# Optimization experiments

Hardware: AMD Instinct MI355X
Metric: run time of the kernel (lower is better)

## Reference

```python
import jax, jax.numpy as jnp
import numpy as np

LOG2_HASHMAP_SIZE = 19
HASHMAP_MASK = np.uint32((1 << LOG2_HASHMAP_SIZE) - 1)
# num_mf_layers=4 -> mf_layer_indices=[2,5,8,11] of the 12-level geometric
# resolution list between base=16 and finest=512
RESOLUTIONS = (30, 80, 210, 512)
PRIMES = (np.uint32(1), np.uint32(11614769), np.uint32(2654435761))
N_POINTS = 2_000_000
N_FEATS = 2

# 8 corner offsets of a 3D voxel, shape [8, 3]
CORNER_OFFSETS = jnp.array([[i, j, k] for i in (0, 1) for j in (0, 1) for k in (0, 1)], dtype=jnp.int32)


def _hash3(coords):
    # coords: [..., 3] int32 grid coordinates -> [...] int32 hash index
    c = coords.astype(jnp.uint32)
    h = (c[..., 0] * PRIMES[0]) ^ (c[..., 1] * PRIMES[1]) ^ (c[..., 2] * PRIMES[2])
    return (h & HASHMAP_MASK).astype(jnp.int32)


def setup_inputs() -> dict:
    key = jax.random.key(0)
    k1, k2 = jax.random.split(key)
    # points inside the unit bounding box
    x = jax.random.uniform(k1, (N_POINTS, 3), dtype=jnp.float32)
    # 4 hash tables, init U(-1e-4, 1e-4) as in nn.init.uniform_
    tables = jax.random.uniform(k2, (len(RESOLUTIONS), 1 << LOG2_HASHMAP_SIZE, N_FEATS),
                                minval=-1e-4, maxval=1e-4, dtype=jnp.float32)
    return {"x": x, "tables": tables}


def reference(x, tables):
    # x: [N, 3] in [0, 1]; tables: [L, 2^19, F]
    outs = []
    for li, res in enumerate(RESOLUTIONS):
        scaled = x * jnp.float32(res)          # [N, 3]
        bottom = jnp.floor(scaled)             # voxel min vertex
        t = scaled - bottom                    # relative position in voxel, [N, 3]
        corners = bottom.astype(jnp.int32)[:, None, :] + CORNER_OFFSETS[None]  # [N, 8, 3]
        idx = _hash3(corners)                  # [N, 8]
        emb = tables[li][idx]                  # gather corner embeddings, [N, 8, F]
        # trilinear weights: prod over dims of (t if offset==1 else 1-t)
        w = jnp.where(CORNER_OFFSETS[None].astype(bool), t[:, None, :], 1.0 - t[:, None, :]).prod(axis=-1)  # [N, 8]
        outs.append(jnp.einsum('nc,ncf->nf', w, emb))  # [N, F]
    return jnp.concatenate(outs, axis=-1)  # [N, L*F] = [N, 8]
```

## Files before the change

### kernel.cpp

```cpp
#include <hip/hip_runtime.h>
#include <hip/hip_fp16.h>
#include <stdint.h>

#define LOG2_HASHMAP_SIZE 19
#define HASHMAP_SIZE (1u << LOG2_HASHMAP_SIZE)
#define HASHMAP_MASK (HASHMAP_SIZE - 1u)
#define N_LEVELS 4

#define R0 31
#define DENSE0_N (R0 * R0 * R0)
#define DENSE0_BYTES (DENSE0_N * 4)

typedef float v4f __attribute__((ext_vector_type(4)));

__device__ __forceinline__ uint32_t hash3(uint32_t ix, uint32_t iy, uint32_t iz) {
    return (ix ^ (iy * 11614769u) ^ (iz * 2654435761u)) & HASHMAP_MASK;
}

__device__ __forceinline__ float2 h2f(uint32_t p) {
    return __half22float2(*(const __half2*)&p);
}
__device__ __forceinline__ uint32_t f2h(float a, float b) {
    const __half2 p = __floats2half2_rn(a, b);
    return *(const uint32_t*)&p;
}

__device__ __forceinline__ float2 level_embed_p(float px, float py, float pz,
                                                const float* __restrict__ tables,
                                                int li, float r)
{
    const uint32_t P1 = 11614769u;
    const uint32_t P2 = 2654435761u;

    const float sx = px * r, sy = py * r, sz = pz * r;
    const float bx = floorf(sx), by = floorf(sy), bz = floorf(sz);
    const float tx = sx - bx, ty = sy - by, tz = sz - bz;
    const float ux = 1.0f - tx, uy = 1.0f - ty, uz = 1.0f - tz;

    const uint32_t ix = (uint32_t)(int)bx;
    const uint32_t iy = (uint32_t)(int)by;
    const uint32_t iz = (uint32_t)(int)bz;

    const uint32_t hy0 = iy * P1, hy1 = (iy + 1u) * P1;
    const uint32_t hz0 = iz * P2, hz1 = (iz + 1u) * P2;

    uint32_t S[4];
    float W[4];
    S[0] = hy0 ^ hz0;  W[0] = uy * uz;
    S[1] = hy0 ^ hz1;  W[1] = uy * tz;
    S[2] = hy1 ^ hz0;  W[2] = ty * uz;
    S[3] = hy1 ^ hz1;  W[3] = ty * tz;

    const float* tab = tables + (size_t)li * HASHMAP_SIZE * 2;
    const float2* __restrict__ tab2 = (const float2*)tab;

    float f0 = 0.0f, f1 = 0.0f;
    #pragma unroll
    for (int c = 0; c < 4; ++c) {
        const uint32_t h0 = (ix ^ S[c]) & HASHMAP_MASK;
        const uint32_t h1 = ((ix + 1u) ^ S[c]) & HASHMAP_MASK;
        const float2 e0 = tab2[h0];
        const float2 e1 = tab2[h1];
        f0 += W[c] * (ux * e0.x + tx * e1.x);
        f1 += W[c] * (ux * e0.y + tx * e1.y);
    }
    return make_float2(f0, f1);
}

__device__ __forceinline__ float2 level_embed_h16(float px, float py, float pz,
                                                  const uint32_t* __restrict__ t16,
                                                  float r)
{
    const uint32_t P1 = 11614769u;
    const uint32_t P2 = 2654435761u;

    const float sx = px * r, sy = py * r, sz = pz * r;
    const float bx = floorf(sx), by = floorf(sy), bz = floorf(sz);
    const float tx = sx - bx, ty = sy - by, tz = sz - bz;
    const float ux = 1.0f - tx, uy = 1.0f - ty, uz = 1.0f - tz;

    const uint32_t ix = (uint32_t)(int)bx;
    const uint32_t iy = (uint32_t)(int)by;
    const uint32_t iz = (uint32_t)(int)bz;

    const uint32_t hy0 = iy * P1, hy1 = (iy + 1u) * P1;
    const uint32_t hz0 = iz * P2, hz1 = (iz + 1u) * P2;

    uint32_t S[4];
    float W[4];
    S[0] = hy0 ^ hz0;  W[0] = uy * uz;
    S[1] = hy0 ^ hz1;  W[1] = uy * tz;
    S[2] = hy1 ^ hz0;  W[2] = ty * uz;
    S[3] = hy1 ^ hz1;  W[3] = ty * tz;

    const uint32_t D = ix ^ (ix + 1u);

    float f0 = 0.0f, f1 = 0.0f;
    if (D == 1u) {
        #pragma unroll
        for (int c = 0; c < 4; ++c) {
            const uint32_t h0 = (ix ^ S[c]) & HASHMAP_MASK;
            const uint2 v = ((const uint2*)t16)[h0 >> 1];
            const uint32_t p0 = (h0 & 1u) ? v.y : v.x;
            const uint32_t p1 = (h0 & 1u) ? v.x : v.y;
            const float2 e0 = h2f(p0);
            const float2 e1 = h2f(p1);
            f0 += W[c] * (ux * e0.x + tx * e1.x);
            f1 += W[c] * (ux * e0.y + tx * e1.y);
        }
    } else if (D == 3u) {
        #pragma unroll
        for (int c = 0; c < 4; ++c) {
            const uint32_t h0 = (ix ^ S[c]) & HASHMAP_MASK;
            const uint32_t b = h0 & ~3u;
            const uint4 v = *(const uint4*)(t16 + b);
            const uint32_t i0 = h0 & 3u;
            const uint32_t s01 = (i0 & 1u) ? v.y : v.x;
            const uint32_t s23 = (i0 & 1u) ? v.w : v.z;
            const uint32_t p0  = (i0 & 2u) ? s23 : s01;
            const uint32_t r01 = (i0 & 1u) ? v.z : v.w;
            const uint32_t r23 = (i0 & 1u) ? v.x : v.y;
            const uint32_t p1  = (i0 & 2u) ? r23 : r01;
            const float2 e0 = h2f(p0);
            const float2 e1 = h2f(p1);
            f0 += W[c] * (ux * e0.x + tx * e1.x);
            f1 += W[c] * (ux * e0.y + tx * e1.y);
        }
    } else {
        #pragma unroll
        for (int c = 0; c < 4; ++c) {
            const uint32_t h0 = (ix ^ S[c]) & HASHMAP_MASK;
            const uint32_t h1 = h0 ^ D;
            const float2 e0 = h2f(t16[h0]);
            const float2 e1 = h2f(t16[h1]);
            f0 += W[c] * (ux * e0.x + tx * e1.x);
            f1 += W[c] * (ux * e0.y + tx * e1.y);
        }
    }
    return make_float2(f0, f1);
}

__global__ __launch_bounds__(256) void convert_fp16(
    const float* __restrict__ tables, uint32_t* __restrict__ t16)
{
    const int i = blockIdx.x * blockDim.x + threadIdx.x;
    if (i >= 3 * (int)HASHMAP_SIZE) return;
    const float2 e = ((const float2*)tables)[HASHMAP_SIZE + i];
    t16[i] = f2h(e.x, e.y);
}

__global__ __launch_bounds__(256) void build_dense0(
    const float* __restrict__ tables, uint32_t* __restrict__ dense0)
{
    const int v = blockIdx.x * blockDim.x + threadIdx.x;
    if (v >= DENSE0_N) return;
    const int vx = v / (R0 * R0);
    const int rem = v - vx * (R0 * R0);
    const int vy = rem / R0;
    const int vz = rem - vy * R0;
    const uint32_t h = hash3((uint32_t)vx, (uint32_t)vy, (uint32_t)vz);
    const float2 e = ((const float2*)tables)[h];
    dense0[v] = f2h(e.x, e.y);
}

__global__ __launch_bounds__(256) void pass_hash(
    const float* __restrict__ x, const uint32_t* __restrict__ t16,
    uint32_t* __restrict__ ws, float r, int n)
{
    const int i = blockIdx.x * blockDim.x + threadIdx.x;
    if (i >= n) return;
    const float px = __builtin_nontemporal_load(x + 3 * (size_t)i + 0);
    const float py = __builtin_nontemporal_load(x + 3 * (size_t)i + 1);
    const float pz = __builtin_nontemporal_load(x + 3 * (size_t)i + 2);
    const float2 e = level_embed_h16(px, py, pz, t16, r);
    __builtin_nontemporal_store(f2h(e.x, e.y), ws + i);
}

extern __shared__ uint32_t s_dense[];

__global__ __launch_bounds__(1024) void final16_kernel(
    const float* __restrict__ x, const uint32_t* __restrict__ t16_l3,
    const uint32_t* __restrict__ dense0,
    const uint32_t* __restrict__ ws1, const uint32_t* __restrict__ ws2,
    float* __restrict__ out, int n)
{
    for (int i = threadIdx.x; i < DENSE0_N; i += 1024)
        s_dense[i] = dense0[i];
    __syncthreads();

    const size_t stride = (size_t)gridDim.x * 1024;
    for (size_t i = (size_t)blockIdx.x * 1024 + threadIdx.x; i < (size_t)n; i += stride) {
        const float px = __builtin_nontemporal_load(x + 3 * i + 0);
        const float py = __builtin_nontemporal_load(x + 3 * i + 1);
        const float pz = __builtin_nontemporal_load(x + 3 * i + 2);

        const float2 e3 = level_embed_h16(px, py, pz, t16_l3, 512.0f);

        const float sx = px * 30.0f, sy = py * 30.0f, sz = pz * 30.0f;
        const float bx = floorf(sx), by = floorf(sy), bz = floorf(sz);
        const float tx = sx - bx, ty = sy - by, tz = sz - bz;
        const float uxv = 1.0f - tx, uyv = 1.0f - ty, uzv = 1.0f - tz;
        const int ix = (int)bx, iy = (int)by, iz = (int)bz;
        const int lin = (ix * R0 + iy) * R0 + iz;

        float f0 = 0.0f, f1 = 0.0f;
        #pragma unroll
        for (int dx = 0; dx < 2; ++dx) {
            const float wx = dx ? tx : uxv;
            #pragma unroll
            for (int dy = 0; dy < 2; ++dy) {
                const float wxy = wx * (dy ? ty : uyv);
                const int base = lin + (dx * R0 + dy) * R0;
                const float2 c0 = h2f(s_dense[base]);
                const float2 c1 = h2f(s_dense[base + 1]);
                f0 += wxy * (uzv * c0.x + tz * c1.x);
                f1 += wxy * (uzv * c0.y + tz * c1.y);
            }
        }

        const float2 e1 = h2f(__builtin_nontemporal_load(ws1 + i));
        const float2 e2 = h2f(__builtin_nontemporal_load(ws2 + i));

        v4f* op = (v4f*)(out + 8 * i);
        v4f lo = {f0, f1, e1.x, e1.y};
        v4f hi = {e2.x, e2.y, e3.x, e3.y};
        __builtin_nontemporal_store(lo, op);
        __builtin_nontemporal_store(hi, op + 1);
    }
}

__global__ __launch_bounds__(256) void pass_direct_kernel(
    const float* __restrict__ x, const float* __restrict__ tables,
    float* __restrict__ out, int li, float r, int n)
{
    const int i = blockIdx.x * blockDim.x + threadIdx.x;
    if (i >= n) return;
    const float px = x[3 * (size_t)i + 0];
    const float py = x[3 * (size_t)i + 1];
    const float pz = x[3 * (size_t)i + 2];
    const float2 e = level_embed_p(px, py, pz, tables, li, r);
    float2* op = (float2*)(out + 8 * (size_t)i + 2 * li);
    *op = e;
}

extern "C" void kernel_launch(void* const* d_in, const int* in_sizes, int n_in,
                              void* d_out, int out_size, void* d_ws, size_t ws_size,
                              hipStream_t stream) {
    const float* x = (const float*)d_in[0];
    const float* tables = (const float*)d_in[1];
    float* out = (float*)d_out;
    const int n = in_sizes[0] / 3;

    const size_t t16_bytes = 3 * (size_t)HASHMAP_SIZE * 4;
    const size_t off_d0    = t16_bytes;
    const size_t off_ws1   = off_d0 + DENSE0_BYTES;
    const size_t off_ws2   = off_ws1 + (size_t)n * 4;
    const size_t ws_needed = off_ws2 + (size_t)n * 4;

    bool fused_ok = (ws_size >= ws_needed);
    if (fused_ok) {
        static int attr_ok = -1;
        if (attr_ok < 0) {
            attr_ok = (hipFuncSetAttribute(
                           reinterpret_cast<const void*>(final16_kernel),
                           hipFuncAttributeMaxDynamicSharedMemorySize,
                           DENSE0_BYTES) == hipSuccess) ? 1 : 0;
        }
        fused_ok = (attr_ok == 1);
    }

    if (fused_ok) {
        char* wsb = (char*)d_ws;
        uint32_t* t16    = (uint32_t*)wsb;
        uint32_t* dense0 = (uint32_t*)(wsb + off_d0);
        uint32_t* ws1    = (uint32_t*)(wsb + off_ws1);
        uint32_t* ws2    = (uint32_t*)(wsb + off_ws2);

        convert_fp16<<<(3 * HASHMAP_SIZE + 255) / 256, 256, 0, stream>>>(tables, t16);
        build_dense0<<<(DENSE0_N + 255) / 256, 256, 0, stream>>>(tables, dense0);

        const int block = 256;
        const int grid = (n + block - 1) / block;
        pass_hash<<<grid, block, 0, stream>>>(x, t16, ws1, 80.0f, n);
        pass_hash<<<grid, block, 0, stream>>>(x, t16 + HASHMAP_SIZE, ws2, 210.0f, n);
        final16_kernel<<<256, 1024, DENSE0_BYTES, stream>>>(
            x, t16 + 2 * HASHMAP_SIZE, dense0, ws1, ws2, out, n);
    } else {
        const float res[N_LEVELS] = {30.0f, 80.0f, 210.0f, 512.0f};
        const int block = 256;
        const int grid = (n + block - 1) / block;
        for (int li = 0; li < N_LEVELS; ++li) {
            pass_direct_kernel<<<grid, block, 0, stream>>>(
                x, tables, out, li, res[li], n);
        }
    }
}
```

Baseline: 239.4 us.

## Merge setup kernels, read level-0 dense grid from global, simplify hash-pair loads

The two table-preparation kernels become one launch. The final kernel no longer copies the 119 KB level-0 dense grid into LDS per block; it reads it from global/L2 with paired 8-byte loads and runs as a plain 256-thread grid instead of a persistent 1024-thread grid. The hashed-level corner lookup drops the 4-wide vector path and splits only on ix parity, fetching an adjacent pair in one load when ix is even. This removes the per-block LDS fill and its occupancy limit, at the cost of L2 traffic for the dense grid and separate loads in the odd-ix case.

New measurement: 253.3 us. +5.8%, slower.

```diff
diff --git a/kernel.cpp b/kernel.cpp
--- a/kernel.cpp
+++ b/kernel.cpp
@@ -11,6 +11,8 @@
 #define DENSE0_N (R0 * R0 * R0)
 #define DENSE0_BYTES (DENSE0_N * 4)
 
+#define CONV_N (3 * (int)HASHMAP_SIZE)
+
 typedef float v4f __attribute__((ext_vector_type(4)));
 
 __device__ __forceinline__ uint32_t hash3(uint32_t ix, uint32_t iy, uint32_t iz) {
@@ -23,6 +25,12 @@
 __device__ __forceinline__ uint32_t f2h(float a, float b) {
     const __half2 p = __floats2half2_rn(a, b);
     return *(const uint32_t*)&p;
+}
+
+__device__ __forceinline__ uint2 load8u(const uint32_t* p) {
+    uint2 v;
+    __builtin_memcpy(&v, p, 8);
+    return v;
 }
 
 __device__ __forceinline__ float2 level_embed_p(float px, float py, float pz,
@@ -93,10 +101,8 @@
     S[2] = hy1 ^ hz0;  W[2] = ty * uz;
     S[3] = hy1 ^ hz1;  W[3] = ty * tz;
 
-    const uint32_t D = ix ^ (ix + 1u);
-
     float f0 = 0.0f, f1 = 0.0f;
-    if (D == 1u) {
+    if ((ix & 1u) == 0u) {
         #pragma unroll
         for (int c = 0; c < 4; ++c) {
             const uint32_t h0 = (ix ^ S[c]) & HASHMAP_MASK;
@@ -108,29 +114,11 @@
             f0 += W[c] * (ux * e0.x + tx * e1.x);
             f1 += W[c] * (ux * e0.y + tx * e1.y);
         }
-    } else if (D == 3u) {
-        #pragma unroll
-        for (int c = 0; c < 4; ++c) {
-            const uint32_t h0 = (ix ^ S[c]) & HASHMAP_MASK;
-            const uint32_t b = h0 & ~3u;
-            const uint4 v = *(const uint4*)(t16 + b);
-            const uint32_t i0 = h0 & 3u;
-            const uint32_t s01 = (i0 & 1u) ? v.y : v.x;
-            const uint32_t s23 = (i0 & 1u) ? v.w : v.z;
-            const uint32_t p0  = (i0 & 2u) ? s23 : s01;
-            const uint32_t r01 = (i0 & 1u) ? v.z : v.w;
-            const uint32_t r23 = (i0 & 1u) ? v.x : v.y;
-            const uint32_t p1  = (i0 & 2u) ? r23 : r01;
-            const float2 e0 = h2f(p0);
-            const float2 e1 = h2f(p1);
-            f0 += W[c] * (ux * e0.x + tx * e1.x);
-            f1 += W[c] * (ux * e0.y + tx * e1.y);
-        }
     } else {
         #pragma unroll
         for (int c = 0; c < 4; ++c) {
             const uint32_t h0 = (ix ^ S[c]) & HASHMAP_MASK;
-            const uint32_t h1 = h0 ^ D;
+            const uint32_t h1 = ((ix + 1u) ^ S[c]) & HASHMAP_MASK;
             const float2 e0 = h2f(t16[h0]);
             const float2 e1 = h2f(t16[h1]);
             f0 += W[c] * (ux * e0.x + tx * e1.x);
@@ -140,27 +128,57 @@
     return make_float2(f0, f1);
 }
 
-__global__ __launch_bounds__(256) void convert_fp16(
-    const float* __restrict__ tables, uint32_t* __restrict__ t16)
-{
-    const int i = blockIdx.x * blockDim.x + threadIdx.x;
-    if (i >= 3 * (int)HASHMAP_SIZE) return;
-    const float2 e = ((const float2*)tables)[HASHMAP_SIZE + i];
-    t16[i] = f2h(e.x, e.y);
-}
-
-__global__ __launch_bounds__(256) void build_dense0(
-    const float* __restrict__ tables, uint32_t* __restrict__ dense0)
-{
-    const int v = blockIdx.x * blockDim.x + threadIdx.x;
-    if (v >= DENSE0_N) return;
-    const int vx = v / (R0 * R0);
-    const int rem = v - vx * (R0 * R0);
-    const int vy = rem / R0;
-    const int vz = rem - vy * R0;
-    const uint32_t h = hash3((uint32_t)vx, (uint32_t)vy, (uint32_t)vz);
-    const float2 e = ((const float2*)tables)[h];
-    dense0[v] = f2h(e.x, e.y);
+__device__ __forceinline__ float2 level0_g(float px, float py, float pz,
+                                           const uint32_t* __restrict__ d0)
+{
+    const float sx = px * 30.0f, sy = py * 30.0f, sz = pz * 30.0f;
+    const float bx = floorf(sx), by = floorf(sy), bz = floorf(sz);
+    const float tx = sx - bx, ty = sy - by, tz = sz - bz;
+    const float ux = 1.0f - tx, uy = 1.0f - ty, uz = 1.0f - tz;
+    const int ix = (int)bx, iy = (int)by, iz = (int)bz;
+    const int lin = (ix * R0 + iy) * R0 + iz;
+
+    float f0 = 0.0f, f1 = 0.0f;
+    #pragma unroll
+    for (int dx = 0; dx < 2; ++dx) {
+        const float wx = dx ? tx : ux;
+        #pragma unroll
+        for (int dy = 0; dy < 2; ++dy) {
+            const float wxy = wx * (dy ? ty : uy);
+            const int base = lin + (dx * R0 + dy) * R0;
+            const uint2 zpair = load8u(d0 + base);
+            const float2 c0 = h2f(zpair.x);
+            const float2 c1 = h2f(zpair.y);
+            f0 += wxy * (uz * c0.x + tz * c1.x);
+            f1 += wxy * (uz * c0.y + tz * c1.y);
+        }
+    }
+    return make_float2(f0, f1);
+}
+
+__global__ __launch_bounds__(256) void setup_all(
+    const float* __restrict__ tables,
+    uint32_t* __restrict__ t16,
+    uint32_t* __restrict__ dense0)
+{
+    int i = blockIdx.x * blockDim.x + threadIdx.x;
+
+    if (i < CONV_N) {
+        const float2 e = ((const float2*)tables)[HASHMAP_SIZE + i];
+        t16[i] = f2h(e.x, e.y);
+        return;
+    }
+    i -= CONV_N;
+
+    if (i < DENSE0_N) {
+        const int vx = i / (R0 * R0);
+        const int rem = i - vx * (R0 * R0);
+        const int vy = rem / R0;
+        const int vz = rem - vy * R0;
+        const uint32_t h = hash3((uint32_t)vx, (uint32_t)vy, (uint32_t)vz);
+        const float2 e = ((const float2*)tables)[h];
+        dense0[i] = f2h(e.x, e.y);
+    }
 }
 
 __global__ __launch_bounds__(256) void pass_hash(
@@ -176,57 +194,29 @@
     __builtin_nontemporal_store(f2h(e.x, e.y), ws + i);
 }
 
-extern __shared__ uint32_t s_dense[];
-
-__global__ __launch_bounds__(1024) void final16_kernel(
+__global__ __launch_bounds__(256) void final_g(
     const float* __restrict__ x, const uint32_t* __restrict__ t16_l3,
     const uint32_t* __restrict__ dense0,
     const uint32_t* __restrict__ ws1, const uint32_t* __restrict__ ws2,
     float* __restrict__ out, int n)
 {
-    for (int i = threadIdx.x; i < DENSE0_N; i += 1024)
-        s_dense[i] = dense0[i];
-    __syncthreads();
-
-    const size_t stride = (size_t)gridDim.x * 1024;
-    for (size_t i = (size_t)blockIdx.x * 1024 + threadIdx.x; i < (size_t)n; i += stride) {
-        const float px = __builtin_nontemporal_load(x + 3 * i + 0);
-        const float py = __builtin_nontemporal_load(x + 3 * i + 1);
-        const float pz = __builtin_nontemporal_load(x + 3 * i + 2);
-
-        const float2 e3 = level_embed_h16(px, py, pz, t16_l3, 512.0f);
-
-        const float sx = px * 30.0f, sy = py * 30.0f, sz = pz * 30.0f;
-        const float bx = floorf(sx), by = floorf(sy), bz = floorf(sz);
-        const float tx = sx - bx, ty = sy - by, tz = sz - bz;
-        const float uxv = 1.0f - tx, uyv = 1.0f - ty, uzv = 1.0f - tz;
-        const int ix = (int)bx, iy = (int)by, iz = (int)bz;
-        const int lin = (ix * R0 + iy) * R0 + iz;
-
-        float f0 = 0.0f, f1 = 0.0f;
-        #pragma unroll
-        for (int dx = 0; dx < 2; ++dx) {
-            const float wx = dx ? tx : uxv;
-            #pragma unroll
-            for (int dy = 0; dy < 2; ++dy) {
-                const float wxy = wx * (dy ? ty : uyv);
-                const int base = lin + (dx * R0 + dy) * R0;
-                const float2 c0 = h2f(s_dense[base]);
-                const float2 c1 = h2f(s_dense[base + 1]);
-                f0 += wxy * (uzv * c0.x + tz * c1.x);
-                f1 += wxy * (uzv * c0.y + tz * c1.y);
-            }
-        }
-
-        const float2 e1 = h2f(__builtin_nontemporal_load(ws1 + i));
-        const float2 e2 = h2f(__builtin_nontemporal_load(ws2 + i));
-
-        v4f* op = (v4f*)(out + 8 * i);
-        v4f lo = {f0, f1, e1.x, e1.y};
-        v4f hi = {e2.x, e2.y, e3.x, e3.y};
-        __builtin_nontemporal_store(lo, op);
-        __builtin_nontemporal_store(hi, op + 1);
-    }
+    const int i = blockIdx.x * blockDim.x + threadIdx.x;
+    if (i >= n) return;
+    const float px = __builtin_nontemporal_load(x + 3 * (size_t)i + 0);
+    const float py = __builtin_nontemporal_load(x + 3 * (size_t)i + 1);
+    const float pz = __builtin_nontemporal_load(x + 3 * (size_t)i + 2);
+
+    const float2 e3 = level_embed_h16(px, py, pz, t16_l3, 512.0f);
+    const float2 e0 = level0_g(px, py, pz, dense0);
+
+    const float2 e1 = h2f(__builtin_nontemporal_load(ws1 + i));
+    const float2 e2 = h2f(__builtin_nontemporal_load(ws2 + i));
+
+    v4f* op = (v4f*)(out + 8 * (size_t)i);
+    v4f lo = {e0.x, e0.y, e1.x, e1.y};
+    v4f hi = {e2.x, e2.y, e3.x, e3.y};
+    __builtin_nontemporal_store(lo, op);
+    __builtin_nontemporal_store(hi, op + 1);
 }
 
 __global__ __launch_bounds__(256) void pass_direct_kernel(
@@ -257,33 +247,22 @@
     const size_t off_ws2   = off_ws1 + (size_t)n * 4;
     const size_t ws_needed = off_ws2 + (size_t)n * 4;
 
-    bool fused_ok = (ws_size >= ws_needed);
-    if (fused_ok) {
-        static int attr_ok = -1;
-        if (attr_ok < 0) {
-            attr_ok = (hipFuncSetAttribute(
-                           reinterpret_cast<const void*>(final16_kernel),
-                           hipFuncAttributeMaxDynamicSharedMemorySize,
-                           DENSE0_BYTES) == hipSuccess) ? 1 : 0;
-        }
-        fused_ok = (attr_ok == 1);
-    }
-
-    if (fused_ok) {
+    if (ws_size >= ws_needed) {
         char* wsb = (char*)d_ws;
         uint32_t* t16    = (uint32_t*)wsb;
         uint32_t* dense0 = (uint32_t*)(wsb + off_d0);
         uint32_t* ws1    = (uint32_t*)(wsb + off_ws1);
         uint32_t* ws2    = (uint32_t*)(wsb + off_ws2);
 
-        convert_fp16<<<(3 * HASHMAP_SIZE + 255) / 256, 256, 0, stream>>>(tables, t16);
-        build_dense0<<<(DENSE0_N + 255) / 256, 256, 0, stream>>>(tables, dense0);
+        const int setup_total = CONV_N + DENSE0_N;
+        setup_all<<<(setup_total + 255) / 256, 256, 0, stream>>>(
+            tables, t16, dense0);
 
         const int block = 256;
         const int grid = (n + block - 1) / block;
         pass_hash<<<grid, block, 0, stream>>>(x, t16, ws1, 80.0f, n);
         pass_hash<<<grid, block, 0, stream>>>(x, t16 + HASHMAP_SIZE, ws2, 210.0f, n);
-        final16_kernel<<<256, 1024, DENSE0_BYTES, stream>>>(
+        final_g<<<grid, block, 0, stream>>>(
             x, t16 + 2 * HASHMAP_SIZE, dense0, ws1, ws2, out, n);
     } else {
         const float res[N_LEVELS] = {30.0f, 80.0f, 210.0f, 512.0f};
```
